# Kernel tuning notes

Measured on AMD Instinct MI355X. Metric: run time of the kernel, lower is better.

The kernel has to match this reference:

```python
import jax, jax.numpy as jnp
import numpy as np

N_NODES = 160_000
N_EDGES = 640_000
N_GRAPHS = 8_000
IN_FEATS = 74
HID = 63
MAX_DEG = 10
PRED_HID = 128
PRED_DIM = 256
BN_EPS = 1e-5
N_LAYERS = 3
PARAM_NAMES = ['W0', 'b0', 'gamma0', 'beta0', 'W1', 'b1', 'gamma1', 'beta1', 'W2', 'b2', 'gamma2', 'beta2', 'W_ng', 'b_ng', 'W_tr', 'b_tr']


def setup_inputs() -> dict:
    key = jax.random.key(0)
    ks = jax.random.split(key, 20)
    inp = {}
    inp['feats'] = jax.random.normal(ks[0], (N_NODES, IN_FEATS), dtype=jnp.float32)
    inp['src'] = jax.random.randint(ks[1], (N_EDGES,), 0, N_NODES, dtype=jnp.int32)
    inp['dst'] = jax.random.randint(ks[2], (N_EDGES,), 0, N_NODES, dtype=jnp.int32)
    # sorted graph membership: 20 nodes per graph (batched molecular graphs)
    inp['graph_ids'] = jnp.repeat(jnp.arange(N_GRAPHS, dtype=jnp.int32), N_NODES // N_GRAPHS)
    dims = [IN_FEATS, HID, HID, HID]
    for l in range(N_LAYERS):
        fi, fo = dims[l], dims[l + 1]
        inp[f'W{l}'] = jax.random.normal(ks[3 + l], (MAX_DEG, fi, fo), dtype=jnp.float32) / np.float32(np.sqrt(fi))
        inp[f'b{l}'] = jnp.zeros((MAX_DEG, fo), dtype=jnp.float32)
        inp[f'gamma{l}'] = jnp.ones((fo,), dtype=jnp.float32)
        inp[f'beta{l}'] = jnp.zeros((fo,), dtype=jnp.float32)
    inp['W_ng'] = jax.random.normal(ks[10], (HID, PRED_HID), dtype=jnp.float32) / np.float32(np.sqrt(HID))
    inp['b_ng'] = jnp.zeros((PRED_HID,), dtype=jnp.float32)
    inp['W_tr'] = jax.random.normal(ks[11], (2 * PRED_HID, PRED_DIM), dtype=jnp.float32) / np.float32(np.sqrt(2 * PRED_HID))
    inp['b_tr'] = jnp.zeros((PRED_DIM,), dtype=jnp.float32)
    return inp


def _nf_layer(h, src, dst, deg_idx, W, b, gamma, beta):
    # message passing: sum of neighbor features via copy_u / fn.sum
    neigh = jax.ops.segment_sum(h[src], dst, num_segments=N_NODES)
    tot = h + neigh  # self + neighbor sum (Duvenaud neural fingerprint)
    # degree-bucketed linear: compute all MAX_DEG transforms, select per node by degree
    z_all = jnp.einsum('ni,kio->nko', tot, W) + b  # [N, MAX_DEG, out]
    z = jnp.take_along_axis(z_all, deg_idx[:, None, None], axis=1)[:, 0, :]  # [N, out]
    z = jax.nn.relu(z)
    # batchnorm over nodes (training-mode batch statistics, eps=1e-5)
    mu = jnp.mean(z, axis=0)
    var = jnp.var(z, axis=0)
    return (z - mu) * jax.lax.rsqrt(var + BN_EPS) * gamma + beta


def _forward(feats, src, dst, graph_ids, params):
    # in-degree per node, clamped to [1, MAX_DEG] -> weight bucket index
    deg = jax.ops.segment_sum(jnp.ones((N_EDGES,), jnp.float32), dst, num_segments=N_NODES)
    deg_idx = jnp.clip(deg.astype(jnp.int32), 1, MAX_DEG) - 1
    h = feats
    for l in range(N_LAYERS):
        h = _nf_layer(h, src, dst, deg_idx, params[f'W{l}'], params[f'b{l}'],
                      params[f'gamma{l}'], params[f'beta{l}'])
    # node_to_graph linear
    h = h @ params['W_ng'] + params['b_ng']  # [N, PRED_HID]
    # SumAndMax readout over each graph
    g_sum = jax.ops.segment_sum(h, graph_ids, num_segments=N_GRAPHS)
    g_max = jax.ops.segment_max(h, graph_ids, num_segments=N_GRAPHS)
    g = jnp.tanh(jnp.concatenate([g_sum, g_max], axis=-1))  # [G, 2*PRED_HID]
    return g @ params['W_tr'] + params['b_tr']  # [G, PRED_DIM]


def reference(feats, src, dst, graph_ids, W0, b0, gamma0, beta0, W1, b1, gamma1, beta1, W2, b2, gamma2, beta2, W_ng, b_ng, W_tr, b_tr):
    params = dict(zip(PARAM_NAMES, (W0, b0, gamma0, beta0, W1, b1, gamma1, beta1, W2, b2, gamma2, beta2, W_ng, b_ng, W_tr, b_tr)))
    return _forward(feats, src, dst, graph_ids, params)
```

## Files before the change

### kernel.cpp

```cpp
#include <hip/hip_runtime.h>
#include <stdint.h>
#include <math.h>

static constexpr int NN = 160000;
static constexpr int NE = 640000;
static constexpr int NG = 8000;
static constexpr int FH  = 63;
static constexpr int ZST = 64;
static constexpr int FST = 80;
static constexpr int NB  = 128;
static constexpr int LGRID = 1536;

static constexpr size_t OFF_DEGCNT = 0;
static constexpr size_t OFF_CURSOR = 640000;
static constexpr size_t OFF_BCNT   = 1280000;
static constexpr size_t OFF_SPART  = 1280064;
static constexpr size_t ZERO_BYTES = 1673280;
static constexpr size_t OFF_ROWPTR = 1673280;
static constexpr size_t OFF_BLKSUM = 2313472;
static constexpr size_t OFF_COL    = 2315520;
static constexpr size_t OFF_BLIST  = 4875520;
static constexpr size_t OFF_AFC    = 17675520;
static constexpr size_t OFF_BNG2   = 17709312;
static constexpr size_t OFF_PBLK   = 17709824;
static constexpr size_t OFF_FB     = 17710080;
static constexpr size_t OFF_Z0     = 43310080;
static constexpr size_t OFF_Z1     = 63790080;
static constexpr size_t OFF_WNGF   = OFF_Z1;
static constexpr size_t OFF_WTRF   = OFF_Z1 + 32768;

__device__ __forceinline__ float blo(unsigned u) {
    union { unsigned i; float f; } v; v.i = u << 16; return v.f;
}
__device__ __forceinline__ float bhi(unsigned u) {
    union { unsigned i; float f; } v; v.i = u & 0xffff0000u; return v.f;
}
__device__ __forceinline__ unsigned short f2b(float f) {
    union { float f; unsigned i; } v; v.f = f;
    unsigned r = v.i + 0x7fffu + ((v.i >> 16) & 1u);
    return (unsigned short)(r >> 16);
}
__device__ __forceinline__ void acc8(float* a, uint4 q) {
    a[0] += blo(q.x); a[1] += bhi(q.x);
    a[2] += blo(q.y); a[3] += bhi(q.y);
    a[4] += blo(q.z); a[5] += bhi(q.z);
    a[6] += blo(q.w); a[7] += bhi(q.w);
}

typedef __attribute__((ext_vector_type(8))) short bf16x8;
typedef __attribute__((ext_vector_type(4))) float f32x4;
union U8 { uint4 u; bf16x8 b; };

__global__ void k_degree(const int* __restrict__ dst, int* __restrict__ degcnt) {
    int e = blockIdx.x * 256 + threadIdx.x;
    if (e < NE) atomicAdd(&degcnt[dst[e]], 1);
}

__global__ void k_scan1(const int* __restrict__ degcnt, int* __restrict__ row_ptr,
                        int* __restrict__ blksum) {
    __shared__ int s[1024];
    int t = threadIdx.x;
    int i = blockIdx.x * 1024 + t;
    int v = (i < NN) ? degcnt[i] : 0;
    s[t] = v; __syncthreads();
    for (int off = 1; off < 1024; off <<= 1) {
        int x = (t >= off) ? s[t - off] : 0;
        __syncthreads();
        s[t] += x;
        __syncthreads();
    }
    if (i < NN) row_ptr[i + 1] = s[t];
    if (t == 1023) blksum[blockIdx.x] = s[t];
}

__global__ void k_scan2(int* __restrict__ blksum, int nblk) {
    __shared__ int s[256];
    int t = threadIdx.x;
    int v = (t < nblk) ? blksum[t] : 0;
    s[t] = v; __syncthreads();
    for (int off = 1; off < 256; off <<= 1) {
        int x = (t >= off) ? s[t - off] : 0;
        __syncthreads();
        s[t] += x;
        __syncthreads();
    }
    if (t < nblk) blksum[t] = s[t] - v;
}

__global__ void k_scan3(int* __restrict__ row_ptr, const int* __restrict__ blksum) {
    int t = threadIdx.x;
    int i = blockIdx.x * 1024 + t;
    if (i < NN) row_ptr[i + 1] += blksum[blockIdx.x];
    if (i == 0) row_ptr[0] = 0;
}

__global__ void k_cast(const float* __restrict__ feats, unsigned short* __restrict__ fb) {
    int i = blockIdx.x * 256 + threadIdx.x;
    if (i >= NN * FST) return;
    int n = i / FST, c = i - n * FST;
    float v = (c < 74) ? feats[n * 74 + c] : 0.f;
    union { float f; unsigned u; } x; x.f = v;
    unsigned r = x.u + 0x7fffu + ((x.u >> 16) & 1u);
    fb[i] = (unsigned short)(r >> 16);
}

__global__ void __launch_bounds__(1024) k_bucket(
        const int* __restrict__ degcnt, const int* __restrict__ row_ptr,
        int* __restrict__ bcnt, int2* __restrict__ blist) {
    __shared__ int scnt[10], sbase[10];
    int tid = threadIdx.x;
    if (tid < 10) scnt[tid] = 0;
    __syncthreads();
    int n = blockIdx.x * 1024 + tid;
    int k = 0, pos = 0;
    bool v = (n < NN);
    int rp = 0;
    if (v) {
        int d = degcnt[n];
        rp = row_ptr[n];
        k = (d < 1) ? 0 : ((d > 10) ? 9 : d - 1);
        pos = atomicAdd(&scnt[k], 1);
    }
    __syncthreads();
    if (tid < 10) sbase[tid] = scnt[tid] ? atomicAdd(&bcnt[tid], scnt[tid]) : 0;
    __syncthreads();
    if (v) blist[k * NN + sbase[k] + pos] = make_int2(n, rp);
}

__global__ void k_prep(const int* __restrict__ bcnt, int* __restrict__ pblk) {
    if (threadIdx.x == 0) {
        int s = 0; pblk[0] = 0;
        for (int k = 0; k < 10; ++k) { s += (bcnt[k] + NB - 1) / NB; pblk[k + 1] = s; }
    }
}

__global__ void k_fill(const int* __restrict__ src, const int* __restrict__ dst,
                       const int* __restrict__ row_ptr, int* __restrict__ cursor,
                       int* __restrict__ col) {
    int e = blockIdx.x * 256 + threadIdx.x;
    if (e >= NE) return;
    int d = dst[e];
    int pos = row_ptr[d] + atomicAdd(&cursor[d], 1);
    col[pos] = src[e];
}

template<int FI, int IST, bool AFF>
__global__ void __launch_bounds__(256, 2) k_layer(
    const unsigned short* __restrict__ in,
    const float* __restrict__ aff,
    const int* __restrict__ row_ptr, const int* __restrict__ col,
    const int* __restrict__ bcnt, const int2* __restrict__ blist,
    const int* __restrict__ pblk,
    const float* __restrict__ W, const float* __restrict__ B,
    unsigned short* __restrict__ zout, float* __restrict__ spart)
{
    constexpr int CH = IST / 8;
    __shared__ float sW[FI * 63 + 64];
    __shared__ float sTot[4][80][8];
    __shared__ int   sN[4][8];
    __shared__ float sRed[2][4][64];

    int b = blockIdx.x;
    if (b >= pblk[10]) return;
    int k = 0;
#pragma unroll
    for (int i = 1; i <= 9; ++i) k += (b >= pblk[i]) ? 1 : 0;
    int base = (b - pblk[k]) * NB;
    int cnt = bcnt[k];
    if (base >= cnt) return;

    int tid = threadIdx.x;
    int wave = tid >> 6, lane = tid & 63;
    int t = lane >> 3, r = lane & 7;

    const float* Wk = W + (size_t)k * FI * 63;
#pragma unroll 4
    for (int i = tid; i < FI * 63; i += 256) sW[i] = Wk[i];
    __syncthreads();

    const uint4* inq = (const uint4*)in;
    float bterm = (lane < 63) ? B[k * 63 + lane] : 0.f;
    float lsum = 0.f, lsq = 0.f;

#pragma unroll 1
    for (int it = 0; it < NB / 32; ++it) {
        int idx = base + it * 32 + wave * 8 + t;
        if (base + it * 32 >= cnt) break;
        bool val = (idx < cnt);
        int2 bl = blist[k * NN + (val ? idx : (cnt - 1))];
        int n = bl.x, rs = bl.y;
        int dg = (k >= 1 && k <= 8) ? (k + 1) : (row_ptr[n + 1] - rs);
        if (r == 0) sN[wave][t] = val ? n : -1;

        float a[8] = {0.f, 0.f, 0.f, 0.f, 0.f, 0.f, 0.f, 0.f};
        {
            uint4 q = inq[(size_t)n * CH + r];
            acc8(a, q);
        }
        int d = 0;
#pragma unroll 1
        for (; d + 4 <= dg; d += 4) {
            int c0 = col[rs + d], c1 = col[rs + d + 1];
            int c2 = col[rs + d + 2], c3 = col[rs + d + 3];
            uint4 q0 = inq[(size_t)c0 * CH + r];
            uint4 q1 = inq[(size_t)c1 * CH + r];
            uint4 q2 = inq[(size_t)c2 * CH + r];
            uint4 q3 = inq[(size_t)c3 * CH + r];
            acc8(a, q0); acc8(a, q1); acc8(a, q2); acc8(a, q3);
        }
#pragma unroll 1
        for (; d < dg; ++d) {
            int c = col[rs + d];
            uint4 q = inq[(size_t)c * CH + r];
            acc8(a, q);
        }

        if constexpr (IST == 80) {
            float e2[8] = {0.f, 0.f, 0.f, 0.f, 0.f, 0.f, 0.f, 0.f};
            if (r < 2) {
                uint4 q = inq[(size_t)n * CH + 8 + r];
                acc8(e2, q);
                int d2 = 0;
#pragma unroll 1
                for (; d2 < dg; ++d2) {
                    int c = col[rs + d2];
                    uint4 p = inq[(size_t)c * CH + 8 + r];
                    acc8(e2, p);
                }
#pragma unroll
                for (int j = 0; j < 8; ++j) sTot[wave][64 + 8 * r + j][t] = e2[j];
            }
        }

        if constexpr (AFF) {
            const float4* af = (const float4*)aff;
            float4 A0 = af[2 * r], A1 = af[2 * r + 1];
            float4 C0 = af[16 + 2 * r], C1 = af[16 + 2 * r + 1];
            float dp1 = (float)(dg + 1);
            a[0] = A0.x * a[0] + dp1 * C0.x;  a[1] = A0.y * a[1] + dp1 * C0.y;
            a[2] = A0.z * a[2] + dp1 * C0.z;  a[3] = A0.w * a[3] + dp1 * C0.w;
            a[4] = A1.x * a[4] + dp1 * C1.x;  a[5] = A1.y * a[5] + dp1 * C1.y;
            a[6] = A1.z * a[6] + dp1 * C1.z;  a[7] = A1.w * a[7] + dp1 * C1.w;
        }

#pragma unroll
        for (int j = 0; j < 8; ++j) sTot[wave][8 * r + j][t] = a[j];

        float acc[8];
#pragma unroll
        for (int i = 0; i < 8; ++i) acc[i] = bterm;
#pragma unroll 4
        for (int j = 0; j < FI; ++j) {
            float w = sW[j * 63 + lane];
            float4 u = *(const float4*)&sTot[wave][j][0];
            float4 v = *(const float4*)&sTot[wave][j][4];
            acc[0] = fmaf(u.x, w, acc[0]); acc[1] = fmaf(u.y, w, acc[1]);
            acc[2] = fmaf(u.z, w, acc[2]); acc[3] = fmaf(u.w, w, acc[3]);
            acc[4] = fmaf(v.x, w, acc[4]); acc[5] = fmaf(v.y, w, acc[5]);
            acc[6] = fmaf(v.z, w, acc[6]); acc[7] = fmaf(v.w, w, acc[7]);
        }

#pragma unroll
        for (int tt = 0; tt < 8; ++tt) {
            int nn = sN[wave][tt];
            float z = fmaxf(acc[tt], 0.f);
            if (nn >= 0 && lane < 63) {
                zout[(size_t)nn * ZST + lane] = f2b(z);
                lsum += z; lsq += z * z;
            }
        }
    }

    sRed[0][wave][lane] = lsum;
    sRed[1][wave][lane] = lsq;
    __syncthreads();
    if (wave == 0 && lane < 63) {
        float s = sRed[0][0][lane] + sRed[0][1][lane] + sRed[0][2][lane] + sRed[0][3][lane];
        float q = sRed[1][0][lane] + sRed[1][1][lane] + sRed[1][2][lane] + sRed[1][3][lane];
        float* sp = spart + (size_t)(blockIdx.x & 255) * 128;
        atomicAdd(&sp[lane], s);
        atomicAdd(&sp[64 + lane], q);
    }
}

__global__ void k_bn(const float* __restrict__ spart, const float* __restrict__ gamma,
                     const float* __restrict__ beta, float* __restrict__ afc) {
    int o = threadIdx.x;
    if (o >= 63) return;
    double s = 0.0, q = 0.0;
    for (int cp = 0; cp < 256; ++cp) {
        s += (double)spart[cp * 128 + o];
        q += (double)spart[cp * 128 + 64 + o];
    }
    double mu  = s / NN;
    double var = q / NN - mu * mu;
    float a = (float)((double)gamma[o] / sqrt(var + 1e-5));
    float c = (float)((double)beta[o] - mu * (double)a);
    afc[o] = a;
    afc[64 + o] = c;
}

__global__ void k_prepw(const float* __restrict__ W_ng, const float* __restrict__ b_ng,
                        const float* __restrict__ afc2, const float* __restrict__ W_tr,
                        unsigned short* __restrict__ WngF, unsigned short* __restrict__ WtrF,
                        float* __restrict__ bng2) {
    int bid = blockIdx.x, tid = threadIdx.x;
    if (bid == 0) {
        if (tid < 128) {
            float acc = b_ng[tid];
            for (int j = 0; j < 63; ++j)
                acc = fmaf(afc2[64 + j], W_ng[j * 128 + tid], acc);
            bng2[tid] = acc;
        }
    } else if (bid <= 64) {
        int idx = (bid - 1) * 256 + tid;
        int j = idx & 7, lane = (idx >> 3) & 63;
        int nt = (idx >> 9) & 7, kb = idx >> 12;
        int k = (kb & 1) * 32 + ((lane >> 4) << 3) + j;
        int col = nt * 16 + (lane & 15);
        float w = (k < 63) ? afc2[k] * W_ng[k * 128 + col] : 0.f;
        unsigned short hi = f2b(w);
        if (kb < 2) WngF[idx] = hi;
        else        WngF[idx] = f2b(w - blo(hi));
    } else {
        int idx = (bid - 65) * 256 + tid;
        int j = idx & 7, lane = (idx >> 3) & 63;
        int kb = (idx >> 9) & 7, nt = idx >> 12;
        int k = kb * 32 + ((lane >> 4) << 3) + j;
        int col = nt * 16 + (lane & 15);
        WtrF[idx] = f2b(W_tr[k * 256 + col]);
    }
}

__global__ void __launch_bounds__(256, 2) k_graph(
    const unsigned short* __restrict__ Z2, const unsigned short* __restrict__ WngF,
    const float* __restrict__ bng2, const unsigned short* __restrict__ WtrF,
    const float* __restrict__ b_tr, float* __restrict__ out)
{
    __shared__ unsigned short sW[16384];
    __shared__ float sT[16 * 256];
    __shared__ float sB[128];

    int tid = threadIdx.x;
    int wave = tid >> 6, lane = tid & 63;
    int gl15 = lane & 15, grp = lane >> 4;

    {
        const uint4* srcq = (const uint4*)WngF;
        uint4* dstq = (uint4*)sW;
#pragma unroll
        for (int i = 0; i < 8; ++i) dstq[tid + 256 * i] = srcq[tid + 256 * i];
    }
    if (tid < 128) sB[tid] = bng2[tid];
    __syncthreads();

    int nodeBase = blockIdx.x * 320 + wave * 80;
    const uint4* zq = (const uint4*)Z2;
    uint4 a0[5], a1[5];
#pragma unroll
    for (int m = 0; m < 5; ++m) {
        size_t row = (size_t)(nodeBase + m * 16 + gl15) * 8;
        a0[m] = zq[row + grp];
        a1[m] = zq[row + 4 + grp];
    }
    if (grp == 3) {
#pragma unroll
        for (int m = 0; m < 5; ++m) a1[m].w &= 0xffffu;
    }

    const uint4* swq = (const uint4*)sW;
    const float NEGI = -3.0e38f;

#pragma unroll 1
    for (int nt = 0; nt < 8; ++nt) {
        U8 b0, b1, b2, b3;
        b0.u = swq[(0 * 8 + nt) * 64 + lane];
        b1.u = swq[(1 * 8 + nt) * 64 + lane];
        b2.u = swq[(2 * 8 + nt) * 64 + lane];
        b3.u = swq[(3 * 8 + nt) * 64 + lane];

        f32x4 ac[5];
#pragma unroll
        for (int m = 0; m < 5; ++m) {
            U8 xa0, xa1; xa0.u = a0[m]; xa1.u = a1[m];
            f32x4 c = {0.f, 0.f, 0.f, 0.f};
            c = __builtin_amdgcn_mfma_f32_16x16x32_bf16(xa0.b, b0.b, c, 0, 0, 0);
            c = __builtin_amdgcn_mfma_f32_16x16x32_bf16(xa1.b, b1.b, c, 0, 0, 0);
            c = __builtin_amdgcn_mfma_f32_16x16x32_bf16(xa0.b, b2.b, c, 0, 0, 0);
            c = __builtin_amdgcn_mfma_f32_16x16x32_bf16(xa1.b, b3.b, c, 0, 0, 0);
            ac[m] = c;
        }

        float s[4] = {0.f, 0.f, 0.f, 0.f};
        float x[4] = {NEGI, NEGI, NEGI, NEGI};
        bool cA = lane < 16, cB = lane < 32, cC = lane < 48;
#pragma unroll
        for (int r = 0; r < 4; ++r) {
            float v0 = ac[0][r]; s[0] += v0; x[0] = fmaxf(x[0], v0);
            float v4 = ac[4][r]; s[3] += v4; x[3] = fmaxf(x[3], v4);
            float v1 = ac[1][r]; float v1a = cA ? v1 : 0.f;
            s[0] += v1a; s[1] += v1 - v1a;
            x[0] = fmaxf(x[0], cA ? v1 : NEGI); x[1] = fmaxf(x[1], cA ? NEGI : v1);
            float v2 = ac[2][r]; float v2a = cB ? v2 : 0.f;
            s[1] += v2a; s[2] += v2 - v2a;
            x[1] = fmaxf(x[1], cB ? v2 : NEGI); x[2] = fmaxf(x[2], cB ? NEGI : v2);
            float v3 = ac[3][r]; float v3a = cC ? v3 : 0.f;
            s[2] += v3a; s[3] += v3 - v3a;
            x[2] = fmaxf(x[2], cC ? v3 : NEGI); x[3] = fmaxf(x[3], cC ? NEGI : v3);
        }
#pragma unroll
        for (int g = 0; g < 4; ++g) {
            s[g] += __shfl_xor(s[g], 16);
            s[g] += __shfl_xor(s[g], 32);
            x[g] = fmaxf(x[g], __shfl_xor(x[g], 16));
            x[g] = fmaxf(x[g], __shfl_xor(x[g], 32));
        }
        if (lane < 16) {
            int c = nt * 16 + lane;
            float bb = sB[c];
#pragma unroll
            for (int g = 0; g < 4; ++g) {
                int row = wave * 4 + g;
                int swz = (row & 7) << 2;
                sT[(row * 256 + c) ^ swz]       = tanhf(s[g] + 20.f * bb);
                sT[(row * 256 + 128 + c) ^ swz] = tanhf(x[g] + bb);
            }
        }
    }
    __syncthreads();

    U8 pa[8];
    {
        int swz = (gl15 & 7) << 2;
#pragma unroll
        for (int kb = 0; kb < 8; ++kb) {
            int k8 = kb * 32 + grp * 8;
            float4 t0 = *(const float4*)&sT[(gl15 * 256 + k8) ^ swz];
            float4 t1 = *(const float4*)&sT[(gl15 * 256 + k8 + 4) ^ swz];
            unsigned u0 = (unsigned)f2b(t0.x) | ((unsigned)f2b(t0.y) << 16);
            unsigned u1 = (unsigned)f2b(t0.z) | ((unsigned)f2b(t0.w) << 16);
            unsigned u2 = (unsigned)f2b(t1.x) | ((unsigned)f2b(t1.y) << 16);
            unsigned u3 = (unsigned)f2b(t1.z) | ((unsigned)f2b(t1.w) << 16);
            pa[kb].u = make_uint4(u0, u1, u2, u3);
        }
    }
    const uint4* wtq = (const uint4*)WtrF;
    size_t gbase = (size_t)blockIdx.x * 16 * 256;
#pragma unroll 2
    for (int i = 0; i < 4; ++i) {
        int nt = wave * 4 + i;
        f32x4 c = {0.f, 0.f, 0.f, 0.f};
#pragma unroll
        for (int kb = 0; kb < 8; ++kb) {
            U8 b; b.u = wtq[(nt * 8 + kb) * 64 + lane];
            c = __builtin_amdgcn_mfma_f32_16x16x32_bf16(pa[kb].b, b.b, c, 0, 0, 0);
        }
        int d = nt * 16 + gl15;
        float btv = b_tr[d];
#pragma unroll
        for (int r = 0; r < 4; ++r) {
            int row = grp * 4 + r;
            out[gbase + (size_t)row * 256 + d] = c[r] + btv;
        }
    }
}

extern "C" void kernel_launch(void* const* d_in, const int* in_sizes, int n_in,
                              void* d_out, int out_size, void* d_ws, size_t ws_size,
                              hipStream_t stream) {
    const float* feats = (const float*)d_in[0];
    const int*   src   = (const int*)d_in[1];
    const int*   dst   = (const int*)d_in[2];
    const float* W0 = (const float*)d_in[4];
    const float* b0 = (const float*)d_in[5];
    const float* g0 = (const float*)d_in[6];
    const float* be0 = (const float*)d_in[7];
    const float* W1 = (const float*)d_in[8];
    const float* b1 = (const float*)d_in[9];
    const float* g1 = (const float*)d_in[10];
    const float* be1 = (const float*)d_in[11];
    const float* W2 = (const float*)d_in[12];
    const float* b2 = (const float*)d_in[13];
    const float* g2 = (const float*)d_in[14];
    const float* be2 = (const float*)d_in[15];
    const float* Wng = (const float*)d_in[16];
    const float* bng = (const float*)d_in[17];
    const float* Wtr = (const float*)d_in[18];
    const float* btr = (const float*)d_in[19];
    float* out = (float*)d_out;

    char* ws = (char*)d_ws;
    int*    degcnt  = (int*)(ws + OFF_DEGCNT);
    int*    cursor  = (int*)(ws + OFF_CURSOR);
    int*    bcnt    = (int*)(ws + OFF_BCNT);
    float*  spart   = (float*)(ws + OFF_SPART);
    int*    row_ptr = (int*)(ws + OFF_ROWPTR);
    int*    blksum  = (int*)(ws + OFF_BLKSUM);
    int*    col     = (int*)(ws + OFF_COL);
    int2*   blist   = (int2*)(ws + OFF_BLIST);
    float*  afc     = (float*)(ws + OFF_AFC);
    float*  bng2    = (float*)(ws + OFF_BNG2);
    int*    pblk    = (int*)(ws + OFF_PBLK);
    unsigned short* Fb = (unsigned short*)(ws + OFF_FB);
    unsigned short* Z0 = (unsigned short*)(ws + OFF_Z0);
    unsigned short* Z1 = (unsigned short*)(ws + OFF_Z1);
    unsigned short* Z2 = Z0;
    unsigned short* WngF = (unsigned short*)(ws + OFF_WNGF);
    unsigned short* WtrF = (unsigned short*)(ws + OFF_WTRF);

    hipMemsetAsync(d_ws, 0, ZERO_BYTES, stream);

    k_degree<<<NE / 256, 256, 0, stream>>>(dst, degcnt);
    k_cast<<<NN * FST / 256, 256, 0, stream>>>(feats, Fb);
    k_scan1<<<157, 1024, 0, stream>>>(degcnt, row_ptr, blksum);
    k_scan2<<<1, 256, 0, stream>>>(blksum, 157);
    k_scan3<<<157, 1024, 0, stream>>>(row_ptr, blksum);
    k_bucket<<<157, 1024, 0, stream>>>(degcnt, row_ptr, bcnt, blist);
    k_prep<<<1, 64, 0, stream>>>(bcnt, pblk);
    k_fill<<<NE / 256, 256, 0, stream>>>(src, dst, row_ptr, cursor, col);

    k_layer<74, FST, false><<<LGRID, 256, 0, stream>>>(
        Fb, nullptr, row_ptr, col, bcnt, blist, pblk, W0, b0, Z0, spart);
    k_bn<<<1, 64, 0, stream>>>(spart, g0, be0, afc);
    k_layer<63, ZST, true><<<LGRID, 256, 0, stream>>>(
        Z0, afc, row_ptr, col, bcnt, blist, pblk, W1, b1, Z1, spart + 256 * 128);
    k_bn<<<1, 64, 0, stream>>>(spart + 256 * 128, g1, be1, afc + 128);
    k_layer<63, ZST, true><<<LGRID, 256, 0, stream>>>(
        Z1, afc + 128, row_ptr, col, bcnt, blist, pblk, W2, b2, Z2, spart + 2 * 256 * 128);
    k_bn<<<1, 64, 0, stream>>>(spart + 2 * 256 * 128, g2, be2, afc + 256);

    k_prepw<<<321, 256, 0, stream>>>(Wng, bng, afc + 256, Wtr, WngF, WtrF, bng2);
    k_graph<<<NG / 16, 256, 0, stream>>>(Z2, WngF, bng2, WtrF, btr, out);
}
```

Before: 450.3 us.

## Software-pipeline neighbor gathers across node batches for fixed-degree buckets

For degree buckets other than the highest, each wave now loads the node metadata and neighbor column indices for all four iterations into shared memory up front. It then issues the register loads for the next batch's self and neighbor feature rows while the current batch runs its dense transform. The goal is to hide gather latency in this latency-bound layer by keeping up to ten uint4 loads in flight per lane. The cost is higher register pressure (q[9] plus prefetch state) and more shared memory. The loop count also becomes a fixed four with no early break, so batches past cnt are processed redundantly.

```diff
diff --git a/kernel.cpp b/kernel.cpp
--- a/kernel.cpp
+++ b/kernel.cpp
@@ -157,7 +157,8 @@
     constexpr int CH = IST / 8;
     __shared__ float sW[FI * 63 + 64];
     __shared__ float sTot[4][80][8];
-    __shared__ int   sN[4][8];
+    __shared__ int   sN[4][4][8];
+    __shared__ int   sCol[4][4][8][9];
     __shared__ float sRed[2][4][64];
 
     int b = blockIdx.x;
@@ -182,91 +183,189 @@
     float bterm = (lane < 63) ? B[k * 63 + lane] : 0.f;
     float lsum = 0.f, lsq = 0.f;
 
+    if (k == 9) {
 #pragma unroll 1
-    for (int it = 0; it < NB / 32; ++it) {
-        int idx = base + it * 32 + wave * 8 + t;
-        if (base + it * 32 >= cnt) break;
-        bool val = (idx < cnt);
-        int2 bl = blist[k * NN + (val ? idx : (cnt - 1))];
-        int n = bl.x, rs = bl.y;
-        int dg = (k >= 1 && k <= 8) ? (k + 1) : (row_ptr[n + 1] - rs);
-        if (r == 0) sN[wave][t] = val ? n : -1;
-
-        float a[8] = {0.f, 0.f, 0.f, 0.f, 0.f, 0.f, 0.f, 0.f};
+        for (int it = 0; it < NB / 32; ++it) {
+            int idx = base + it * 32 + wave * 8 + t;
+            if (base + it * 32 >= cnt) break;
+            bool val = (idx < cnt);
+            int2 bl = blist[k * NN + (val ? idx : (cnt - 1))];
+            int n = bl.x, rs = bl.y;
+            int dg = row_ptr[n + 1] - rs;
+            if (r == 0) sN[wave][it][t] = val ? n : -1;
+
+            float a[8] = {0.f, 0.f, 0.f, 0.f, 0.f, 0.f, 0.f, 0.f};
+            {
+                uint4 q = inq[(size_t)n * CH + r];
+                acc8(a, q);
+            }
+            int d = 0;
+#pragma unroll 1
+            for (; d + 4 <= dg; d += 4) {
+                int c0 = col[rs + d], c1 = col[rs + d + 1];
+                int c2 = col[rs + d + 2], c3 = col[rs + d + 3];
+                uint4 q0 = inq[(size_t)c0 * CH + r];
+                uint4 q1 = inq[(size_t)c1 * CH + r];
+                uint4 q2 = inq[(size_t)c2 * CH + r];
+                uint4 q3 = inq[(size_t)c3 * CH + r];
+                acc8(a, q0); acc8(a, q1); acc8(a, q2); acc8(a, q3);
+            }
+#pragma unroll 1
+            for (; d < dg; ++d) {
+                int c = col[rs + d];
+                uint4 q = inq[(size_t)c * CH + r];
+                acc8(a, q);
+            }
+
+            if constexpr (IST == 80) {
+                float e2[8] = {0.f, 0.f, 0.f, 0.f, 0.f, 0.f, 0.f, 0.f};
+                if (r < 2) {
+                    uint4 q = inq[(size_t)n * CH + 8 + r];
+                    acc8(e2, q);
+                    int d2 = 0;
+#pragma unroll 1
+                    for (; d2 < dg; ++d2) {
+                        int c = col[rs + d2];
+                        uint4 p = inq[(size_t)c * CH + 8 + r];
+                        acc8(e2, p);
+                    }
+#pragma unroll
+                    for (int j = 0; j < 8; ++j) sTot[wave][64 + 8 * r + j][t] = e2[j];
+                }
+            }
+
+            if constexpr (AFF) {
+                const float4* af = (const float4*)aff;
+                float4 A0 = af[2 * r], A1 = af[2 * r + 1];
+                float4 C0 = af[16 + 2 * r], C1 = af[16 + 2 * r + 1];
+                float dp1 = (float)(dg + 1);
+                a[0] = A0.x * a[0] + dp1 * C0.x;  a[1] = A0.y * a[1] + dp1 * C0.y;
+                a[2] = A0.z * a[2] + dp1 * C0.z;  a[3] = A0.w * a[3] + dp1 * C0.w;
+                a[4] = A1.x * a[4] + dp1 * C1.x;  a[5] = A1.y * a[5] + dp1 * C1.y;
+                a[6] = A1.z * a[6] + dp1 * C1.z;  a[7] = A1.w * a[7] + dp1 * C1.w;
+            }
+
+#pragma unroll
+            for (int j = 0; j < 8; ++j) sTot[wave][8 * r + j][t] = a[j];
+
+            float acc[8];
+#pragma unroll
+            for (int i = 0; i < 8; ++i) acc[i] = bterm;
+#pragma unroll 4
+            for (int j = 0; j < FI; ++j) {
+                float w = sW[j * 63 + lane];
+                float4 u = *(const float4*)&sTot[wave][j][0];
+                float4 v = *(const float4*)&sTot[wave][j][4];
+                acc[0] = fmaf(u.x, w, acc[0]); acc[1] = fmaf(u.y, w, acc[1]);
+                acc[2] = fmaf(u.z, w, acc[2]); acc[3] = fmaf(u.w, w, acc[3]);
+                acc[4] = fmaf(v.x, w, acc[4]); acc[5] = fmaf(v.y, w, acc[5]);
+                acc[6] = fmaf(v.z, w, acc[6]); acc[7] = fmaf(v.w, w, acc[7]);
+            }
+
+#pragma unroll
+            for (int tt = 0; tt < 8; ++tt) {
+                int nn = sN[wave][it][tt];
+                float z = fmaxf(acc[tt], 0.f);
+                if (nn >= 0 && lane < 63) {
+                    zout[(size_t)nn * ZST + lane] = f2b(z);
+                    lsum += z; lsq += z * z;
+                }
+            }
+        }
+    } else {
+        int nn_[4], dg_[4];
         {
-            uint4 q = inq[(size_t)n * CH + r];
-            acc8(a, q);
-        }
-        int d = 0;
-#pragma unroll 1
-        for (; d + 4 <= dg; d += 4) {
-            int c0 = col[rs + d], c1 = col[rs + d + 1];
-            int c2 = col[rs + d + 2], c3 = col[rs + d + 3];
-            uint4 q0 = inq[(size_t)c0 * CH + r];
-            uint4 q1 = inq[(size_t)c1 * CH + r];
-            uint4 q2 = inq[(size_t)c2 * CH + r];
-            uint4 q3 = inq[(size_t)c3 * CH + r];
-            acc8(a, q0); acc8(a, q1); acc8(a, q2); acc8(a, q3);
-        }
-#pragma unroll 1
-        for (; d < dg; ++d) {
-            int c = col[rs + d];
-            uint4 q = inq[(size_t)c * CH + r];
-            acc8(a, q);
-        }
-
-        if constexpr (IST == 80) {
-            float e2[8] = {0.f, 0.f, 0.f, 0.f, 0.f, 0.f, 0.f, 0.f};
-            if (r < 2) {
-                uint4 q = inq[(size_t)n * CH + 8 + r];
-                acc8(e2, q);
-                int d2 = 0;
-#pragma unroll 1
-                for (; d2 < dg; ++d2) {
-                    int c = col[rs + d2];
-                    uint4 p = inq[(size_t)c * CH + 8 + r];
+            int rs_[4];
+#pragma unroll
+            for (int it = 0; it < 4; ++it) {
+                int idx = base + it * 32 + wave * 8 + t;
+                bool val = (idx < cnt);
+                int2 bl = blist[k * NN + (val ? idx : (cnt - 1))];
+                nn_[it] = bl.x; rs_[it] = bl.y;
+                dg_[it] = (k >= 1) ? (k + 1) : (row_ptr[bl.x + 1] - bl.y);
+                if (r == 0) sN[wave][it][t] = val ? bl.x : -1;
+            }
+#pragma unroll
+            for (int it = 0; it < 4; ++it) {
+                if (r < dg_[it]) sCol[wave][it][t][r] = col[rs_[it] + r];
+                if (r == 0 && dg_[it] > 8) sCol[wave][it][t][8] = col[rs_[it] + 8];
+            }
+        }
+
+        uint4 qs, q[9];
+        qs = inq[(size_t)nn_[0] * CH + r];
+#pragma unroll
+        for (int d = 0; d < 9; ++d)
+            if (d < dg_[0]) q[d] = inq[(size_t)sCol[wave][0][t][d] * CH + r];
+
+#pragma unroll
+        for (int it = 0; it < 4; ++it) {
+            int dg = dg_[it];
+            float a[8] = {0.f, 0.f, 0.f, 0.f, 0.f, 0.f, 0.f, 0.f};
+            acc8(a, qs);
+#pragma unroll
+            for (int d = 0; d < 9; ++d)
+                if (d < dg) acc8(a, q[d]);
+
+            if (it < 3) {
+                qs = inq[(size_t)nn_[it + 1] * CH + r];
+#pragma unroll
+                for (int d = 0; d < 9; ++d)
+                    if (d < dg_[it + 1]) q[d] = inq[(size_t)sCol[wave][it + 1][t][d] * CH + r];
+            }
+
+            if constexpr (IST == 80) {
+                float e2[8] = {0.f, 0.f, 0.f, 0.f, 0.f, 0.f, 0.f, 0.f};
+                if (r < 2) {
+                    uint4 p = inq[(size_t)nn_[it] * CH + 8 + r];
                     acc8(e2, p);
+#pragma unroll
+                    for (int d2 = 0; d2 < 9; ++d2)
+                        if (d2 < dg) {
+                            uint4 p2 = inq[(size_t)sCol[wave][it][t][d2] * CH + 8 + r];
+                            acc8(e2, p2);
+                        }
+#pragma unroll
+                    for (int j = 0; j < 8; ++j) sTot[wave][64 + 8 * r + j][t] = e2[j];
                 }
-#pragma unroll
-                for (int j = 0; j < 8; ++j) sTot[wave][64 + 8 * r + j][t] = e2[j];
-            }
-        }
-
-        if constexpr (AFF) {
-            const float4* af = (const float4*)aff;
-            float4 A0 = af[2 * r], A1 = af[2 * r + 1];
-            float4 C0 = af[16 + 2 * r], C1 = af[16 + 2 * r + 1];
-            float dp1 = (float)(dg + 1);
-            a[0] = A0.x * a[0] + dp1 * C0.x;  a[1] = A0.y * a[1] + dp1 * C0.y;
-            a[2] = A0.z * a[2] + dp1 * C0.z;  a[3] = A0.w * a[3] + dp1 * C0.w;
-            a[4] = A1.x * a[4] + dp1 * C1.x;  a[5] = A1.y * a[5] + dp1 * C1.y;
-            a[6] = A1.z * a[6] + dp1 * C1.z;  a[7] = A1.w * a[7] + dp1 * C1.w;
-        }
-
-#pragma unroll
-        for (int j = 0; j < 8; ++j) sTot[wave][8 * r + j][t] = a[j];
-
-        float acc[8];
-#pragma unroll
-        for (int i = 0; i < 8; ++i) acc[i] = bterm;
+            }
+
+            if constexpr (AFF) {
+                const float4* af = (const float4*)aff;
+                float4 A0 = af[2 * r], A1 = af[2 * r + 1];
+                float4 C0 = af[16 + 2 * r], C1 = af[16 + 2 * r + 1];
+                float dp1 = (float)(dg + 1);
+                a[0] = A0.x * a[0] + dp1 * C0.x;  a[1] = A0.y * a[1] + dp1 * C0.y;
+                a[2] = A0.z * a[2] + dp1 * C0.z;  a[3] = A0.w * a[3] + dp1 * C0.w;
+                a[4] = A1.x * a[4] + dp1 * C1.x;  a[5] = A1.y * a[5] + dp1 * C1.y;
+                a[6] = A1.z * a[6] + dp1 * C1.z;  a[7] = A1.w * a[7] + dp1 * C1.w;
+            }
+
+#pragma unroll
+            for (int j = 0; j < 8; ++j) sTot[wave][8 * r + j][t] = a[j];
+
+            float acc[8];
+#pragma unroll
+            for (int i = 0; i < 8; ++i) acc[i] = bterm;
 #pragma unroll 4
-        for (int j = 0; j < FI; ++j) {
-            float w = sW[j * 63 + lane];
-            float4 u = *(const float4*)&sTot[wave][j][0];
-            float4 v = *(const float4*)&sTot[wave][j][4];
-            acc[0] = fmaf(u.x, w, acc[0]); acc[1] = fmaf(u.y, w, acc[1]);
-            acc[2] = fmaf(u.z, w, acc[2]); acc[3] = fmaf(u.w, w, acc[3]);
-            acc[4] = fmaf(v.x, w, acc[4]); acc[5] = fmaf(v.y, w, acc[5]);
-            acc[6] = fmaf(v.z, w, acc[6]); acc[7] = fmaf(v.w, w, acc[7]);
-        }
-
-#pragma unroll
-        for (int tt = 0; tt < 8; ++tt) {
-            int nn = sN[wave][tt];
-            float z = fmaxf(acc[tt], 0.f);
-            if (nn >= 0 && lane < 63) {
-                zout[(size_t)nn * ZST + lane] = f2b(z);
-                lsum += z; lsq += z * z;
+            for (int j = 0; j < FI; ++j) {
+                float w = sW[j * 63 + lane];
+                float4 u = *(const float4*)&sTot[wave][j][0];
+                float4 v = *(const float4*)&sTot[wave][j][4];
+                acc[0] = fmaf(u.x, w, acc[0]); acc[1] = fmaf(u.y, w, acc[1]);
+                acc[2] = fmaf(u.z, w, acc[2]); acc[3] = fmaf(u.w, w, acc[3]);
+                acc[4] = fmaf(v.x, w, acc[4]); acc[5] = fmaf(v.y, w, acc[5]);
+                acc[6] = fmaf(v.z, w, acc[6]); acc[7] = fmaf(v.w, w, acc[7]);
+            }
+
+#pragma unroll
+            for (int tt = 0; tt < 8; ++tt) {
+                int nn = sN[wave][it][tt];
+                float z = fmaxf(acc[tt], 0.f);
+                if (nn >= 0 && lane < 63) {
+                    zout[(size_t)nn * ZST + lane] = f2b(z);
+                    lsum += z; lsq += z * z;
+                }
             }
         }
     }
```

After: 510.4 us. 13.4% more time.
